# Optimization experiments

Hardware: AMD Instinct MI355X
Metric: run time of the kernel (lower is better)

The kernel has to match this reference:

```python
import jax, jax.numpy as jnp
import numpy as np

B, C, H, W = 8, 256, 64, 64
CQK = C // 8  # query/key channels = 32


def setup_inputs() -> dict:
    key = jax.random.key(0)
    ks = jax.random.split(key, 9)
    s_in = 1.0 / np.sqrt(C)  # conv2d default init scale (kernel_size=1)
    x = jax.random.normal(ks[0], (B, C, H, W), dtype=jnp.float32)
    Wq = jax.random.uniform(ks[1], (CQK, C), jnp.float32, -s_in, s_in)
    bq = jax.random.uniform(ks[2], (CQK,), jnp.float32, -s_in, s_in)
    Wk = jax.random.uniform(ks[3], (CQK, C), jnp.float32, -s_in, s_in)
    bk = jax.random.uniform(ks[4], (CQK,), jnp.float32, -s_in, s_in)
    Wv = jax.random.uniform(ks[5], (C, C), jnp.float32, -s_in, s_in)
    bv = jax.random.uniform(ks[6], (C,), jnp.float32, -s_in, s_in)
    Wf = jax.random.uniform(ks[7], (C, C), jnp.float32, -s_in, s_in)
    bf = jax.random.uniform(ks[8], (C,), jnp.float32, -s_in, s_in)
    return {"x": x, "Wq": Wq, "bq": bq, "Wk": Wk, "bk": bk,
            "Wv": Wv, "bv": bv, "Wf": Wf, "bf": bf}


def reference(x, Wq, bq, Wk, bk, Wv, bv, Wf, bf):
    b, c, h, w = x.shape
    n = h * w
    xf = x.reshape(b, c, n)  # [B, C, N]  (1x1 conv == channel matmul)
    q = jnp.einsum('oc,bcn->bon', Wq, xf) + bq[None, :, None]  # [B, C/8, N]
    k = jnp.einsum('oc,bcn->bon', Wk, xf) + bk[None, :, None]  # [B, C/8, N]
    v = jnp.einsum('oc,bcn->bon', Wv, xf) + bv[None, :, None]  # [B, C, N]
    # energy[b,i,j] = sum_c q[b,c,i] * k[b,c,j]; no scaling (matches source)
    energy = jnp.einsum('bci,bcj->bij', q, k)  # [B, N, N]
    attn = jax.nn.softmax(energy, axis=-1)
    # out[b,c,i] = sum_j v[b,c,j] * attn[b,i,j]
    out = jnp.einsum('bcj,bij->bci', v, attn)  # [B, C, N]
    out = jnp.einsum('oc,bcn->bon', Wf, out) + bf[None, :, None]
    return out.reshape(b, c, h, w)
```

## Files before the change

### kernel.cpp

```cpp
#include <hip/hip_runtime.h>
#include <hip/hip_bf16.h>

#define BATCH 8
#define CCH   256
#define NPOS  4096
#define CQK   32

typedef __attribute__((ext_vector_type(8))) short short8;
typedef __attribute__((ext_vector_type(4))) float f32x4;

__device__ inline unsigned short f2b(float f) {
    __hip_bfloat16 h = __float2bfloat16(f);
    return *reinterpret_cast<unsigned short*>(&h);
}

__device__ inline size_t qk_addr(int b, int n, int c) {
    return ((((size_t)b * 256 + (n >> 4)) * 4 + (c >> 3)) * 16 + (n & 15)) * 8 + (c & 7);
}
__device__ inline size_t v_addr(int b, int c, int j) {
    return (((((size_t)b * 128 + (j >> 5)) * 16 + (c >> 4)) * 4 + ((j >> 3) & 3)) * 16 + (c & 15)) * 8 + (j & 7);
}
__device__ inline size_t wsw_addr(int og, int c, int ol) {
    return ((size_t)(og * 8 + (c >> 5))) * 512 + (((c >> 3) & 3) * 16 + ol) * 8 + (c & 7);
}

__global__ __launch_bounds__(256, 4)
void prep_w_kernel(const float* __restrict__ Wq, const float* __restrict__ Wk,
                   const float* __restrict__ Wv, const float* __restrict__ Wf,
                   unsigned short* __restrict__ wsw)
{
    const int og = blockIdx.x;
    const int t  = threadIdx.x;
    const float* src; int orow;
    if (og < 2)       { src = Wq; orow = og * 16; }
    else if (og < 4)  { src = Wk; orow = (og - 2) * 16; }
    else if (og < 20) { src = Wv; orow = (og - 4) * 16; }
    else              { src = Wf; orow = (og - 20) * 16; }
    #pragma unroll
    for (int e = 0; e < 16; ++e) {
        int idx = t + e * 256;
        int ol = idx >> 8, c = idx & 255;
        wsw[wsw_addr(og, c, ol)] = f2b(src[(orow + ol) * 256 + c]);
    }
}

__global__ __launch_bounds__(512, 2)
void qkv_kernel(const float* __restrict__ x,
                const unsigned short* __restrict__ wsw,
                const float* __restrict__ bq, const float* __restrict__ bk,
                const float* __restrict__ bv,
                unsigned short* __restrict__ qb, unsigned short* __restrict__ kb,
                unsigned short* __restrict__ vb)
{
    __shared__ __align__(16) unsigned short xl[64 * 280];

    const int nt   = blockIdx.x;
    const int b    = blockIdx.y;
    const int t    = threadIdx.x;
    const int w    = t >> 6;
    const int lane = t & 63;
    const int q    = lane >> 4;
    const int ln   = lane & 15;
    const int lofs = (q * 16 + ln) * 8;
    const int wq   = w & 3;
    const int ith  = w >> 2;

    {
        const int c  = t & 255;
        const int nb = (t >> 8) * 4;
        const float* xb = x + ((size_t)(b * 256 + c)) * 4096 + nt * 64;
        #pragma unroll
        for (int e = 0; e < 8; ++e) {
            const int n = nb + e * 8;
            float4 v = *(const float4*)(xb + n);
            xl[(n + 0) * 280 + c] = f2b(v.x);
            xl[(n + 1) * 280 + c] = f2b(v.y);
            xl[(n + 2) * 280 + c] = f2b(v.z);
            xl[(n + 3) * 280 + c] = f2b(v.w);
        }
    }
    __syncthreads();

    short8 wqk[8];
    #pragma unroll
    for (int kk = 0; kk < 8; ++kk)
        wqk[kk] = *(const short8*)(wsw + (size_t)(wq * 8 + kk) * 512 + lofs);
    const float* bias = (wq < 2) ? bq : bk;
    const int cb16 = (wq & 1) * 16;
    const float b0 = bias[cb16 + q * 4 + 0];
    const float b1 = bias[cb16 + q * 4 + 1];
    const float b2 = bias[cb16 + q * 4 + 2];
    const float b3 = bias[cb16 + q * 4 + 3];
    unsigned short* dst = (wq < 2) ? qb : kb;

    #pragma unroll
    for (int itl = 0; itl < 2; ++itl) {
        const int it = ith * 2 + itl;
        short8 xf[8];
        #pragma unroll
        for (int kk = 0; kk < 8; ++kk)
            xf[kk] = *(const short8*)&xl[(it * 16 + ln) * 280 + kk * 32 + q * 8];

        {
            f32x4 acc = {b0, b1, b2, b3};
            #pragma unroll
            for (int kk = 0; kk < 8; ++kk)
                acc = __builtin_amdgcn_mfma_f32_16x16x32_bf16(wqk[kk], xf[kk], acc, 0, 0, 0);
            ushort4 s = {f2b(acc[0]), f2b(acc[1]), f2b(acc[2]), f2b(acc[3])};
            *(ushort4*)(dst + qk_addr(b, nt * 64 + it * 16 + ln, cb16 + q * 4)) = s;
        }

        #pragma unroll
        for (int oq = 0; oq < 4; ++oq) {
            const int c  = wq * 64 + oq * 16 + ln;
            const float bb = bv[c];
            f32x4 acc = {bb, bb, bb, bb};
            const int og = 4 + wq * 4 + oq;
            #pragma unroll
            for (int kk = 0; kk < 8; ++kk) {
                short8 bfr = *(const short8*)(wsw + (size_t)(og * 8 + kk) * 512 + lofs);
                acc = __builtin_amdgcn_mfma_f32_16x16x32_bf16(xf[kk], bfr, acc, 0, 0, 0);
            }
            ushort4 s = {f2b(acc[0]), f2b(acc[1]), f2b(acc[2]), f2b(acc[3])};
            *(ushort4*)(vb + v_addr(b, c, nt * 64 + it * 16 + q * 4)) = s;
        }
    }
}

__global__ __launch_bounds__(256, 2)
void attn_kernel(const unsigned short* __restrict__ qb,
                 const unsigned short* __restrict__ kb,
                 const unsigned short* __restrict__ vb,
                 const unsigned short* __restrict__ wsw,
                 const float* __restrict__ bfb, float* __restrict__ out)
{
    __shared__ __align__(16) unsigned short shbuf[64 * 264];
    __shared__ float lred[64];

    const int bid  = blockIdx.x;
    const int b    = bid & 7;
    const int i0   = (bid >> 3) * 64;
    const int t    = threadIdx.x;
    const int w    = t >> 6;
    const int lane = t & 63;
    const int quad = lane >> 4;
    const int ln   = lane & 15;

    const int ibase = i0 + w * 16;
    const int lofs  = (quad * 16 + ln) * 8;
    const unsigned pswz = (unsigned)((ln & 7) << 4);

    const short8 qfrag = *(const short8*)(qb + (((size_t)b * 256 + (ibase >> 4)) * 512) + lofs);

    f32x4 acc[4][4];
    #pragma unroll
    for (int it = 0; it < 4; ++it)
        #pragma unroll
        for (int cc = 0; cc < 4; ++cc) acc[it][cc] = (f32x4){0.f, 0.f, 0.f, 0.f};
    float accl = 0.f;

    const unsigned short* kbase = kb + (size_t)b * 256 * 512;
    const unsigned short* vbase = vb + (size_t)b * 128 * 8192;

    short8 kf[4], vf[4][2];
    #pragma unroll
    for (int jc = 0; jc < 4; ++jc)
        kf[jc] = *(const short8*)(kbase + (size_t)jc * 512 + lofs);
    #pragma unroll
    for (int cc = 0; cc < 4; ++cc) {
        vf[cc][0] = *(const short8*)(vbase + (w * 4 + cc) * 512 + lofs);
        vf[cc][1] = *(const short8*)(vbase + 8192 + (w * 4 + cc) * 512 + lofs);
    }

    int pb = 0;
    for (int j0 = 0; j0 < 4096; j0 += 64, pb ^= 1) {
        const int jn = (j0 + 64) & 4095;
        short8 kf_n[4], vf_n[4][2];
        #pragma unroll
        for (int jc = 0; jc < 4; ++jc)
            kf_n[jc] = *(const short8*)(kbase + ((size_t)((jn >> 4) + jc) * 512) + lofs);
        const unsigned short* vt_n = vbase + (size_t)(jn >> 5) * 8192;
        #pragma unroll
        for (int cc = 0; cc < 4; ++cc) {
            vf_n[cc][0] = *(const short8*)(vt_n + (w * 4 + cc) * 512 + lofs);
            vf_n[cc][1] = *(const short8*)(vt_n + 8192 + (w * 4 + cc) * 512 + lofs);
        }
        f32x4 st[4];
        #pragma unroll
        for (int jc = 0; jc < 4; ++jc)
            st[jc] = __builtin_amdgcn_mfma_f32_16x16x32_bf16(kf[jc], qfrag,
                      (f32x4){0.f, 0.f, 0.f, 0.f}, 0, 0, 0);
        #pragma unroll
        for (int jc = 0; jc < 4; ++jc) {
            float p0 = __expf(st[jc][0]);
            float p1 = __expf(st[jc][1]);
            float p2 = __expf(st[jc][2]);
            float p3 = __expf(st[jc][3]);
            accl += (p0 + p1) + (p2 + p3);
            ushort4 pk = {f2b(p0), f2b(p1), f2b(p2), f2b(p3)};
            unsigned byt = (((unsigned)(pb * 64 + w * 16 + ln)) << 7)
                         + ((jc * 32 + quad * 8) ^ pswz);
            *(ushort4*)((unsigned char*)shbuf + byt) = pk;
        }
        __syncthreads();
        #pragma unroll
        for (int it = 0; it < 4; ++it) {
            const unsigned rowb = ((unsigned)(pb * 64 + it * 16 + ln)) << 7;
            const short8 pf0 = *(const short8*)((const unsigned char*)shbuf
                                 + rowb + ((quad * 16) ^ pswz));
            const short8 pf1 = *(const short8*)((const unsigned char*)shbuf
                                 + rowb + ((64 + quad * 16) ^ pswz));
            #pragma unroll
            for (int cc = 0; cc < 4; ++cc) {
                acc[it][cc] = __builtin_amdgcn_mfma_f32_16x16x32_bf16(pf0, vf[cc][0], acc[it][cc], 0, 0, 0);
                acc[it][cc] = __builtin_amdgcn_mfma_f32_16x16x32_bf16(pf1, vf[cc][1], acc[it][cc], 0, 0, 0);
            }
        }
        #pragma unroll
        for (int jc = 0; jc < 4; ++jc) kf[jc] = kf_n[jc];
        #pragma unroll
        for (int cc = 0; cc < 4; ++cc) {
            vf[cc][0] = vf_n[cc][0];
            vf[cc][1] = vf_n[cc][1];
        }
    }

    {
        float v = accl;
        v += __shfl_xor(v, 16, 64);
        v += __shfl_xor(v, 32, 64);
        if (lane < 16) lred[w * 16 + lane] = v;
    }
    __syncthreads();

    #pragma unroll
    for (int it = 0; it < 4; ++it) {
        float linv[4];
        #pragma unroll
        for (int r = 0; r < 4; ++r) linv[r] = 1.f / lred[it * 16 + quad * 4 + r];
        #pragma unroll
        for (int cc = 0; cc < 4; ++cc) {
            const int c = w * 64 + cc * 16 + ln;
            #pragma unroll
            for (int r = 0; r < 4; ++r)
                shbuf[((size_t)(it * 16 + quad * 4 + r)) * 264 + c] = f2b(acc[it][cc][r] * linv[r]);
        }
    }
    __syncthreads();

    #pragma unroll
    for (int it = 0; it < 4; ++it) {
        short8 af[8];
        #pragma unroll
        for (int kk = 0; kk < 8; ++kk)
            af[kk] = *(const short8*)&shbuf[((size_t)(it * 16 + ln)) * 264 + kk * 32 + quad * 8];
        #pragma unroll
        for (int oq = 0; oq < 4; ++oq) {
            const int o  = w * 64 + oq * 16 + ln;
            const int og = 20 + w * 4 + oq;
            f32x4 pa = {0.f, 0.f, 0.f, 0.f};
            #pragma unroll
            for (int kk = 0; kk < 8; ++kk) {
                short8 bfr = *(const short8*)(wsw + (size_t)(og * 8 + kk) * 512 + lofs);
                pa = __builtin_amdgcn_mfma_f32_16x16x32_bf16(af[kk], bfr, pa, 0, 0, 0);
            }
            const float bias = bfb[o];
            float4 s = {pa[0] + bias, pa[1] + bias, pa[2] + bias, pa[3] + bias};
            *(float4*)(out + (size_t)(b * 256 + o) * 4096 + i0 + it * 16 + quad * 4) = s;
        }
    }
}

extern "C" void kernel_launch(void* const* d_in, const int* in_sizes, int n_in,
                              void* d_out, int out_size, void* d_ws, size_t ws_size,
                              hipStream_t stream)
{
    const float* x  = (const float*)d_in[0];
    const float* Wq = (const float*)d_in[1];
    const float* bq = (const float*)d_in[2];
    const float* Wk = (const float*)d_in[3];
    const float* bk = (const float*)d_in[4];
    const float* Wv = (const float*)d_in[5];
    const float* bv = (const float*)d_in[6];
    const float* Wf = (const float*)d_in[7];
    const float* bf = (const float*)d_in[8];
    float* out = (float*)d_out;

    unsigned short* qb  = (unsigned short*)d_ws;
    unsigned short* kb  = qb + (size_t)BATCH * NPOS * CQK;
    unsigned short* vb  = kb + (size_t)BATCH * NPOS * CQK;
    unsigned short* wsw = vb + (size_t)BATCH * CCH * NPOS;

    prep_w_kernel<<<36, 256, 0, stream>>>(Wq, Wk, Wv, Wf, wsw);
    qkv_kernel<<<dim3(64, 8), 512, 0, stream>>>(x, wsw, bq, bk, bv, qb, kb, vb);
    attn_kernel<<<512, 256, 0, stream>>>(qb, kb, vb, wsw, bf, out);
}
```

Measured before the change: 203.9 us.

## Fuse weight prep, QKV projection and attention into one persistent kernel with grid barrier

Measured after the change: 334.0 us. 1.64x slower.

```diff
diff --git a/kernel.cpp b/kernel.cpp
--- a/kernel.cpp
+++ b/kernel.cpp
@@ -14,143 +14,138 @@
     return *reinterpret_cast<unsigned short*>(&h);
 }
 
+__device__ inline short8 pack8(float4 a, float4 b) {
+    short8 s;
+    ((unsigned short*)&s)[0] = f2b(a.x);
+    ((unsigned short*)&s)[1] = f2b(a.y);
+    ((unsigned short*)&s)[2] = f2b(a.z);
+    ((unsigned short*)&s)[3] = f2b(a.w);
+    ((unsigned short*)&s)[4] = f2b(b.x);
+    ((unsigned short*)&s)[5] = f2b(b.y);
+    ((unsigned short*)&s)[6] = f2b(b.z);
+    ((unsigned short*)&s)[7] = f2b(b.w);
+    return s;
+}
+
 __device__ inline size_t qk_addr(int b, int n, int c) {
     return ((((size_t)b * 256 + (n >> 4)) * 4 + (c >> 3)) * 16 + (n & 15)) * 8 + (c & 7);
 }
 __device__ inline size_t v_addr(int b, int c, int j) {
     return (((((size_t)b * 128 + (j >> 5)) * 16 + (c >> 4)) * 4 + ((j >> 3) & 3)) * 16 + (c & 15)) * 8 + (j & 7);
 }
-__device__ inline size_t wsw_addr(int og, int c, int ol) {
-    return ((size_t)(og * 8 + (c >> 5))) * 512 + (((c >> 3) & 3) * 16 + ol) * 8 + (c & 7);
-}
-
-__global__ __launch_bounds__(256, 4)
-void prep_w_kernel(const float* __restrict__ Wq, const float* __restrict__ Wk,
-                   const float* __restrict__ Wv, const float* __restrict__ Wf,
-                   unsigned short* __restrict__ wsw)
+
+__global__ __launch_bounds__(256, 2)
+void fused_kernel(const float* __restrict__ x,
+                  const float* __restrict__ Wq, const float* __restrict__ bq,
+                  const float* __restrict__ Wk, const float* __restrict__ bk,
+                  const float* __restrict__ Wv, const float* __restrict__ bv,
+                  const float* __restrict__ Wf, const float* __restrict__ bfb,
+                  unsigned short* __restrict__ kb, unsigned short* __restrict__ vb,
+                  unsigned int* bar, float* __restrict__ out)
 {
-    const int og = blockIdx.x;
-    const int t  = threadIdx.x;
-    const float* src; int orow;
-    if (og < 2)       { src = Wq; orow = og * 16; }
-    else if (og < 4)  { src = Wk; orow = (og - 2) * 16; }
-    else if (og < 20) { src = Wv; orow = (og - 4) * 16; }
-    else              { src = Wf; orow = (og - 20) * 16; }
-    #pragma unroll
-    for (int e = 0; e < 16; ++e) {
-        int idx = t + e * 256;
-        int ol = idx >> 8, c = idx & 255;
-        wsw[wsw_addr(og, c, ol)] = f2b(src[(orow + ol) * 256 + c]);
-    }
-}
-
-__global__ __launch_bounds__(512, 2)
-void qkv_kernel(const float* __restrict__ x,
-                const unsigned short* __restrict__ wsw,
-                const float* __restrict__ bq, const float* __restrict__ bk,
-                const float* __restrict__ bv,
-                unsigned short* __restrict__ qb, unsigned short* __restrict__ kb,
-                unsigned short* __restrict__ vb)
-{
-    __shared__ __align__(16) unsigned short xl[64 * 280];
-
-    const int nt   = blockIdx.x;
-    const int b    = blockIdx.y;
+    __shared__ __align__(16) unsigned short smem[16896];
+    __shared__ __align__(16) unsigned short qlds[2048];
+    __shared__ float lred[64];
+
+    const int bid  = blockIdx.x;
+    const int b    = bid & 7;
+    const int tile = bid >> 3;
     const int t    = threadIdx.x;
     const int w    = t >> 6;
     const int lane = t & 63;
     const int q    = lane >> 4;
     const int ln   = lane & 15;
     const int lofs = (q * 16 + ln) * 8;
-    const int wq   = w & 3;
-    const int ith  = w >> 2;
 
     {
-        const int c  = t & 255;
-        const int nb = (t >> 8) * 4;
-        const float* xb = x + ((size_t)(b * 256 + c)) * 4096 + nt * 64;
-        #pragma unroll
-        for (int e = 0; e < 8; ++e) {
-            const int n = nb + e * 8;
-            float4 v = *(const float4*)(xb + n);
-            xl[(n + 0) * 280 + c] = f2b(v.x);
-            xl[(n + 1) * 280 + c] = f2b(v.y);
-            xl[(n + 2) * 280 + c] = f2b(v.z);
-            xl[(n + 3) * 280 + c] = f2b(v.w);
-        }
-    }
-    __syncthreads();
-
-    short8 wqk[8];
-    #pragma unroll
-    for (int kk = 0; kk < 8; ++kk)
-        wqk[kk] = *(const short8*)(wsw + (size_t)(wq * 8 + kk) * 512 + lofs);
-    const float* bias = (wq < 2) ? bq : bk;
-    const int cb16 = (wq & 1) * 16;
-    const float b0 = bias[cb16 + q * 4 + 0];
-    const float b1 = bias[cb16 + q * 4 + 1];
-    const float b2 = bias[cb16 + q * 4 + 2];
-    const float b3 = bias[cb16 + q * 4 + 3];
-    unsigned short* dst = (wq < 2) ? qb : kb;
-
-    #pragma unroll
-    for (int itl = 0; itl < 2; ++itl) {
-        const int it = ith * 2 + itl;
-        short8 xf[8];
+        const float* xb = x + ((size_t)b * 256) * 4096 + tile * 64;
+        #pragma unroll
+        for (int e = 0; e < 16; ++e) {
+            const int g  = e * 256 + t;
+            const int c  = g >> 4;
+            const int n4 = (g & 15) * 4;
+            float4 v = *(const float4*)(xb + (size_t)c * 4096 + n4);
+            ushort4 s4 = {f2b(v.x), f2b(v.y), f2b(v.z), f2b(v.w)};
+            *(ushort4*)&smem[c * 66 + n4] = s4;
+        }
+        short8 wqk[8];
+        const float* wsrc = ((w < 2) ? Wq : Wk)
+                          + (size_t)((w & 1) * 16 + ln) * 256 + q * 8;
         #pragma unroll
         for (int kk = 0; kk < 8; ++kk)
-            xf[kk] = *(const short8*)&xl[(it * 16 + ln) * 280 + kk * 32 + q * 8];
-
-        {
-            f32x4 acc = {b0, b1, b2, b3};
-            #pragma unroll
-            for (int kk = 0; kk < 8; ++kk)
-                acc = __builtin_amdgcn_mfma_f32_16x16x32_bf16(wqk[kk], xf[kk], acc, 0, 0, 0);
-            ushort4 s = {f2b(acc[0]), f2b(acc[1]), f2b(acc[2]), f2b(acc[3])};
-            *(ushort4*)(dst + qk_addr(b, nt * 64 + it * 16 + ln, cb16 + q * 4)) = s;
-        }
-
-        #pragma unroll
-        for (int oq = 0; oq < 4; ++oq) {
-            const int c  = wq * 64 + oq * 16 + ln;
-            const float bb = bv[c];
-            f32x4 acc = {bb, bb, bb, bb};
-            const int og = 4 + wq * 4 + oq;
-            #pragma unroll
-            for (int kk = 0; kk < 8; ++kk) {
-                short8 bfr = *(const short8*)(wsw + (size_t)(og * 8 + kk) * 512 + lofs);
-                acc = __builtin_amdgcn_mfma_f32_16x16x32_bf16(xf[kk], bfr, acc, 0, 0, 0);
+            wqk[kk] = pack8(*(const float4*)(wsrc + kk * 32),
+                            *(const float4*)(wsrc + kk * 32 + 4));
+        const float* bias = (w < 2) ? bq : bk;
+        const int cb16 = (w & 1) * 16;
+        const float b0 = bias[cb16 + q * 4 + 0];
+        const float b1 = bias[cb16 + q * 4 + 1];
+        const float b2 = bias[cb16 + q * 4 + 2];
+        const float b3 = bias[cb16 + q * 4 + 3];
+        __syncthreads();
+
+        #pragma unroll
+        for (int oqh = 0; oqh < 2; ++oqh) {
+            short8 vwf[2][8];
+            float  bvv[2];
+            #pragma unroll
+            for (int oq2 = 0; oq2 < 2; ++oq2) {
+                const int row = w * 64 + (oqh * 2 + oq2) * 16 + ln;
+                bvv[oq2] = bv[row];
+                const float* vs = Wv + (size_t)row * 256 + q * 8;
+                #pragma unroll
+                for (int kk = 0; kk < 8; ++kk)
+                    vwf[oq2][kk] = pack8(*(const float4*)(vs + kk * 32),
+                                         *(const float4*)(vs + kk * 32 + 4));
             }
-            ushort4 s = {f2b(acc[0]), f2b(acc[1]), f2b(acc[2]), f2b(acc[3])};
-            *(ushort4*)(vb + v_addr(b, c, nt * 64 + it * 16 + q * 4)) = s;
-        }
-    }
-}
-
-__global__ __launch_bounds__(256, 2)
-void attn_kernel(const unsigned short* __restrict__ qb,
-                 const unsigned short* __restrict__ kb,
-                 const unsigned short* __restrict__ vb,
-                 const unsigned short* __restrict__ wsw,
-                 const float* __restrict__ bfb, float* __restrict__ out)
-{
-    __shared__ __align__(16) unsigned short shbuf[64 * 264];
-    __shared__ float lred[64];
-
-    const int bid  = blockIdx.x;
-    const int b    = bid & 7;
-    const int i0   = (bid >> 3) * 64;
-    const int t    = threadIdx.x;
-    const int w    = t >> 6;
-    const int lane = t & 63;
-    const int quad = lane >> 4;
-    const int ln   = lane & 15;
-
-    const int ibase = i0 + w * 16;
-    const int lofs  = (quad * 16 + ln) * 8;
+            #pragma unroll
+            for (int it = 0; it < 4; ++it) {
+                short8 xf[8];
+                #pragma unroll
+                for (int kk = 0; kk < 8; ++kk) {
+                    short8 s;
+                    #pragma unroll
+                    for (int j = 0; j < 8; ++j)
+                        ((unsigned short*)&s)[j] = smem[(kk * 32 + q * 8 + j) * 66 + it * 16 + ln];
+                    xf[kk] = s;
+                }
+                if (oqh == 0) {
+                    f32x4 acc = {b0, b1, b2, b3};
+                    #pragma unroll
+                    for (int kk = 0; kk < 8; ++kk)
+                        acc = __builtin_amdgcn_mfma_f32_16x16x32_bf16(wqk[kk], xf[kk], acc, 0, 0, 0);
+                    ushort4 s = {f2b(acc[0]), f2b(acc[1]), f2b(acc[2]), f2b(acc[3])};
+                    if (w < 2)
+                        *(ushort4*)(qlds + qk_addr(0, it * 16 + ln, cb16 + q * 4)) = s;
+                    else
+                        *(ushort4*)(kb + qk_addr(b, tile * 64 + it * 16 + ln, cb16 + q * 4)) = s;
+                }
+                #pragma unroll
+                for (int oq2 = 0; oq2 < 2; ++oq2) {
+                    const int c = w * 64 + (oqh * 2 + oq2) * 16 + ln;
+                    f32x4 acc = {bvv[oq2], bvv[oq2], bvv[oq2], bvv[oq2]};
+                    #pragma unroll
+                    for (int kk = 0; kk < 8; ++kk)
+                        acc = __builtin_amdgcn_mfma_f32_16x16x32_bf16(xf[kk], vwf[oq2][kk], acc, 0, 0, 0);
+                    ushort4 s = {f2b(acc[0]), f2b(acc[1]), f2b(acc[2]), f2b(acc[3])};
+                    *(ushort4*)(vb + v_addr(b, c, tile * 64 + it * 16 + q * 4)) = s;
+                }
+            }
+        }
+    }
+
+    __threadfence();
+    __syncthreads();
+    if (t == 0) {
+        atomicAdd(bar, 1u);
+        while (atomicAdd(bar, 0u) < 512u) __builtin_amdgcn_s_sleep(8);
+    }
+    __syncthreads();
+    __threadfence();
+
+    const int i0   = tile * 64;
     const unsigned pswz = (unsigned)((ln & 7) << 4);
 
-    const short8 qfrag = *(const short8*)(qb + (((size_t)b * 256 + (ibase >> 4)) * 512) + lofs);
+    const short8 qfrag = *(const short8*)(qlds + (size_t)w * 512 + lofs);
 
     f32x4 acc[4][4];
     #pragma unroll
@@ -199,17 +194,17 @@
             accl += (p0 + p1) + (p2 + p3);
             ushort4 pk = {f2b(p0), f2b(p1), f2b(p2), f2b(p3)};
             unsigned byt = (((unsigned)(pb * 64 + w * 16 + ln)) << 7)
-                         + ((jc * 32 + quad * 8) ^ pswz);
-            *(ushort4*)((unsigned char*)shbuf + byt) = pk;
+                         + ((jc * 32 + q * 8) ^ pswz);
+            *(ushort4*)((unsigned char*)smem + byt) = pk;
         }
         __syncthreads();
         #pragma unroll
         for (int it = 0; it < 4; ++it) {
             const unsigned rowb = ((unsigned)(pb * 64 + it * 16 + ln)) << 7;
-            const short8 pf0 = *(const short8*)((const unsigned char*)shbuf
-                                 + rowb + ((quad * 16) ^ pswz));
-            const short8 pf1 = *(const short8*)((const unsigned char*)shbuf
-                                 + rowb + ((64 + quad * 16) ^ pswz));
+            const short8 pf0 = *(const short8*)((const unsigned char*)smem
+                                 + rowb + ((q * 16) ^ pswz));
+            const short8 pf1 = *(const short8*)((const unsigned char*)smem
+                                 + rowb + ((64 + q * 16) ^ pswz));
             #pragma unroll
             for (int cc = 0; cc < 4; ++cc) {
                 acc[it][cc] = __builtin_amdgcn_mfma_f32_16x16x32_bf16(pf0, vf[cc][0], acc[it][cc], 0, 0, 0);
@@ -237,36 +232,39 @@
     for (int it = 0; it < 4; ++it) {
         float linv[4];
         #pragma unroll
-        for (int r = 0; r < 4; ++r) linv[r] = 1.f / lred[it * 16 + quad * 4 + r];
+        for (int r = 0; r < 4; ++r) linv[r] = 1.f / lred[it * 16 + q * 4 + r];
         #pragma unroll
         for (int cc = 0; cc < 4; ++cc) {
             const int c = w * 64 + cc * 16 + ln;
             #pragma unroll
             for (int r = 0; r < 4; ++r)
-                shbuf[((size_t)(it * 16 + quad * 4 + r)) * 264 + c] = f2b(acc[it][cc][r] * linv[r]);
-        }
-    }
-    __syncthreads();
-
-    #pragma unroll
-    for (int it = 0; it < 4; ++it) {
-        short8 af[8];
+                smem[((size_t)(it * 16 + q * 4 + r)) * 264 + c] = f2b(acc[it][cc][r] * linv[r]);
+        }
+    }
+    __syncthreads();
+
+    #pragma unroll
+    for (int oq = 0; oq < 4; ++oq) {
+        const int o = w * 64 + oq * 16 + ln;
+        short8 wff[8];
+        const float* fs = Wf + (size_t)o * 256 + q * 8;
         #pragma unroll
         for (int kk = 0; kk < 8; ++kk)
-            af[kk] = *(const short8*)&shbuf[((size_t)(it * 16 + ln)) * 264 + kk * 32 + quad * 8];
-        #pragma unroll
-        for (int oq = 0; oq < 4; ++oq) {
-            const int o  = w * 64 + oq * 16 + ln;
-            const int og = 20 + w * 4 + oq;
+            wff[kk] = pack8(*(const float4*)(fs + kk * 32),
+                            *(const float4*)(fs + kk * 32 + 4));
+        const float bias = bfb[o];
+        #pragma unroll
+        for (int it = 0; it < 4; ++it) {
+            short8 af[8];
+            #pragma unroll
+            for (int kk = 0; kk < 8; ++kk)
+                af[kk] = *(const short8*)&smem[((size_t)(it * 16 + ln)) * 264 + kk * 32 + q * 8];
             f32x4 pa = {0.f, 0.f, 0.f, 0.f};
             #pragma unroll
-            for (int kk = 0; kk < 8; ++kk) {
-                short8 bfr = *(const short8*)(wsw + (size_t)(og * 8 + kk) * 512 + lofs);
-                pa = __builtin_amdgcn_mfma_f32_16x16x32_bf16(af[kk], bfr, pa, 0, 0, 0);
-            }
-            const float bias = bfb[o];
+            for (int kk = 0; kk < 8; ++kk)
+                pa = __builtin_amdgcn_mfma_f32_16x16x32_bf16(af[kk], wff[kk], pa, 0, 0, 0);
             float4 s = {pa[0] + bias, pa[1] + bias, pa[2] + bias, pa[3] + bias};
-            *(float4*)(out + (size_t)(b * 256 + o) * 4096 + i0 + it * 16 + quad * 4) = s;
+            *(float4*)(out + (size_t)(b * 256 + o) * 4096 + i0 + it * 16 + q * 4) = s;
         }
     }
 }
@@ -286,12 +284,11 @@
     const float* bf = (const float*)d_in[8];
     float* out = (float*)d_out;
 
-    unsigned short* qb  = (unsigned short*)d_ws;
-    unsigned short* kb  = qb + (size_t)BATCH * NPOS * CQK;
+    unsigned int*   bar = (unsigned int*)d_ws;
+    unsigned short* kb  = (unsigned short*)d_ws + 64;
     unsigned short* vb  = kb + (size_t)BATCH * NPOS * CQK;
-    unsigned short* wsw = vb + (size_t)BATCH * CCH * NPOS;
-
-    prep_w_kernel<<<36, 256, 0, stream>>>(Wq, Wk, Wv, Wf, wsw);
-    qkv_kernel<<<dim3(64, 8), 512, 0, stream>>>(x, wsw, bq, bk, bv, qb, kb, vb);
-    attn_kernel<<<512, 256, 0, stream>>>(qb, kb, vb, wsw, bf, out);
-}
+
+    hipMemsetAsync(bar, 0, 8, stream);
+    fused_kernel<<<512, 256, 0, stream>>>(x, Wq, bq, Wk, bk, Wv, bv, Wf, bf,
+                                          kb, vb, bar, out);
+}
```

## Software-pipeline attention loop: overlap next tile's softmax with current PV MFMAs

Applied to the files above, without the earlier changes.

New measurement: 213.1 us. +4.5%, slower.

```diff
diff --git a/kernel.cpp b/kernel.cpp
--- a/kernel.cpp
+++ b/kernel.cpp
@@ -5,6 +5,7 @@
 #define CCH   256
 #define NPOS  4096
 #define CQK   32
+#define LOG2E 1.4426950408889634f
 
 typedef __attribute__((ext_vector_type(8))) short short8;
 typedef __attribute__((ext_vector_type(4))) float f32x4;
@@ -31,16 +32,16 @@
 {
     const int og = blockIdx.x;
     const int t  = threadIdx.x;
-    const float* src; int orow;
+    const float* src; int orow; float scl = 1.f;
     if (og < 2)       { src = Wq; orow = og * 16; }
-    else if (og < 4)  { src = Wk; orow = (og - 2) * 16; }
+    else if (og < 4)  { src = Wk; orow = (og - 2) * 16; scl = LOG2E; }
     else if (og < 20) { src = Wv; orow = (og - 4) * 16; }
     else              { src = Wf; orow = (og - 20) * 16; }
     #pragma unroll
     for (int e = 0; e < 16; ++e) {
         int idx = t + e * 256;
         int ol = idx >> 8, c = idx & 255;
-        wsw[wsw_addr(og, c, ol)] = f2b(src[(orow + ol) * 256 + c]);
+        wsw[wsw_addr(og, c, ol)] = f2b(src[(orow + ol) * 256 + c] * scl);
     }
 }
 
@@ -86,11 +87,12 @@
     for (int kk = 0; kk < 8; ++kk)
         wqk[kk] = *(const short8*)(wsw + (size_t)(wq * 8 + kk) * 512 + lofs);
     const float* bias = (wq < 2) ? bq : bk;
+    const float ksc = (wq < 2) ? 1.f : LOG2E;
     const int cb16 = (wq & 1) * 16;
-    const float b0 = bias[cb16 + q * 4 + 0];
-    const float b1 = bias[cb16 + q * 4 + 1];
-    const float b2 = bias[cb16 + q * 4 + 2];
-    const float b3 = bias[cb16 + q * 4 + 3];
+    const float b0 = bias[cb16 + q * 4 + 0] * ksc;
+    const float b1 = bias[cb16 + q * 4 + 1] * ksc;
+    const float b2 = bias[cb16 + q * 4 + 2] * ksc;
+    const float b3 = bias[cb16 + q * 4 + 3] * ksc;
     unsigned short* dst = (wq < 2) ? qb : kb;
 
     #pragma unroll
@@ -162,47 +164,55 @@
     const unsigned short* kbase = kb + (size_t)b * 256 * 512;
     const unsigned short* vbase = vb + (size_t)b * 128 * 8192;
 
-    short8 kf[4], vf[4][2];
+    short8 kfB[4], kfC[4], vfA[4][2], vfB[4][2];
     #pragma unroll
     for (int jc = 0; jc < 4; ++jc)
-        kf[jc] = *(const short8*)(kbase + (size_t)jc * 512 + lofs);
+        kfC[jc] = *(const short8*)(kbase + (size_t)jc * 512 + lofs);
     #pragma unroll
     for (int cc = 0; cc < 4; ++cc) {
-        vf[cc][0] = *(const short8*)(vbase + (w * 4 + cc) * 512 + lofs);
-        vf[cc][1] = *(const short8*)(vbase + 8192 + (w * 4 + cc) * 512 + lofs);
-    }
+        vfA[cc][0] = *(const short8*)(vbase + (w * 4 + cc) * 512 + lofs);
+        vfA[cc][1] = *(const short8*)(vbase + 8192 + (w * 4 + cc) * 512 + lofs);
+    }
+    #pragma unroll
+    for (int jc = 0; jc < 4; ++jc)
+        kfB[jc] = *(const short8*)(kbase + (size_t)(4 + jc) * 512 + lofs);
+
+    #pragma unroll
+    for (int jc = 0; jc < 4; ++jc) {
+        f32x4 st = __builtin_amdgcn_mfma_f32_16x16x32_bf16(kfC[jc], qfrag,
+                    (f32x4){0.f, 0.f, 0.f, 0.f}, 0, 0, 0);
+        float p0 = exp2f(st[0]);
+        float p1 = exp2f(st[1]);
+        float p2 = exp2f(st[2]);
+        float p3 = exp2f(st[3]);
+        accl += (p0 + p1) + (p2 + p3);
+        ushort4 pk = {f2b(p0), f2b(p1), f2b(p2), f2b(p3)};
+        unsigned byt = (((unsigned)(w * 16 + ln)) << 7)
+                     + ((jc * 32 + quad * 8) ^ pswz);
+        *(ushort4*)((unsigned char*)shbuf + byt) = pk;
+    }
+    __syncthreads();
 
     int pb = 0;
-    for (int j0 = 0; j0 < 4096; j0 += 64, pb ^= 1) {
-        const int jn = (j0 + 64) & 4095;
-        short8 kf_n[4], vf_n[4][2];
+    for (int j0 = 0; j0 < 4032; j0 += 64, pb ^= 1) {
+        const int jn1 = j0 + 64;
+        const int jn2 = (j0 + 128) & 4095;
+        const unsigned short* vt = vbase + (size_t)(jn1 >> 5) * 8192;
+        #pragma unroll
+        for (int cc = 0; cc < 4; ++cc) {
+            vfB[cc][0] = *(const short8*)(vt + (w * 4 + cc) * 512 + lofs);
+            vfB[cc][1] = *(const short8*)(vt + 8192 + (w * 4 + cc) * 512 + lofs);
+        }
         #pragma unroll
         for (int jc = 0; jc < 4; ++jc)
-            kf_n[jc] = *(const short8*)(kbase + ((size_t)((jn >> 4) + jc) * 512) + lofs);
-        const unsigned short* vt_n = vbase + (size_t)(jn >> 5) * 8192;
-        #pragma unroll
-        for (int cc = 0; cc < 4; ++cc) {
-            vf_n[cc][0] = *(const short8*)(vt_n + (w * 4 + cc) * 512 + lofs);
-            vf_n[cc][1] = *(const short8*)(vt_n + 8192 + (w * 4 + cc) * 512 + lofs);
-        }
-        f32x4 st[4];
+            kfC[jc] = *(const short8*)(kbase + ((size_t)((jn2 >> 4) + jc) * 512) + lofs);
+
+        __builtin_amdgcn_s_setprio(1);
+        f32x4 stB[4];
         #pragma unroll
         for (int jc = 0; jc < 4; ++jc)
-            st[jc] = __builtin_amdgcn_mfma_f32_16x16x32_bf16(kf[jc], qfrag,
-                      (f32x4){0.f, 0.f, 0.f, 0.f}, 0, 0, 0);
-        #pragma unroll
-        for (int jc = 0; jc < 4; ++jc) {
-            float p0 = __expf(st[jc][0]);
-            float p1 = __expf(st[jc][1]);
-            float p2 = __expf(st[jc][2]);
-            float p3 = __expf(st[jc][3]);
-            accl += (p0 + p1) + (p2 + p3);
-            ushort4 pk = {f2b(p0), f2b(p1), f2b(p2), f2b(p3)};
-            unsigned byt = (((unsigned)(pb * 64 + w * 16 + ln)) << 7)
-                         + ((jc * 32 + quad * 8) ^ pswz);
-            *(ushort4*)((unsigned char*)shbuf + byt) = pk;
-        }
-        __syncthreads();
+            stB[jc] = __builtin_amdgcn_mfma_f32_16x16x32_bf16(kfB[jc], qfrag,
+                       (f32x4){0.f, 0.f, 0.f, 0.f}, 0, 0, 0);
         #pragma unroll
         for (int it = 0; it < 4; ++it) {
             const unsigned rowb = ((unsigned)(pb * 64 + it * 16 + ln)) << 7;
@@ -212,16 +222,44 @@
                                  + rowb + ((64 + quad * 16) ^ pswz));
             #pragma unroll
             for (int cc = 0; cc < 4; ++cc) {
-                acc[it][cc] = __builtin_amdgcn_mfma_f32_16x16x32_bf16(pf0, vf[cc][0], acc[it][cc], 0, 0, 0);
-                acc[it][cc] = __builtin_amdgcn_mfma_f32_16x16x32_bf16(pf1, vf[cc][1], acc[it][cc], 0, 0, 0);
+                acc[it][cc] = __builtin_amdgcn_mfma_f32_16x16x32_bf16(pf0, vfA[cc][0], acc[it][cc], 0, 0, 0);
+                acc[it][cc] = __builtin_amdgcn_mfma_f32_16x16x32_bf16(pf1, vfA[cc][1], acc[it][cc], 0, 0, 0);
             }
         }
-        #pragma unroll
-        for (int jc = 0; jc < 4; ++jc) kf[jc] = kf_n[jc];
+        __builtin_amdgcn_s_setprio(0);
+        #pragma unroll
+        for (int jc = 0; jc < 4; ++jc) {
+            float p0 = exp2f(stB[jc][0]);
+            float p1 = exp2f(stB[jc][1]);
+            float p2 = exp2f(stB[jc][2]);
+            float p3 = exp2f(stB[jc][3]);
+            accl += (p0 + p1) + (p2 + p3);
+            ushort4 pk = {f2b(p0), f2b(p1), f2b(p2), f2b(p3)};
+            unsigned byt = (((unsigned)((pb ^ 1) * 64 + w * 16 + ln)) << 7)
+                         + ((jc * 32 + quad * 8) ^ pswz);
+            *(ushort4*)((unsigned char*)shbuf + byt) = pk;
+        }
+        __syncthreads();
+        #pragma unroll
+        for (int jc = 0; jc < 4; ++jc) kfB[jc] = kfC[jc];
         #pragma unroll
         for (int cc = 0; cc < 4; ++cc) {
-            vf[cc][0] = vf_n[cc][0];
-            vf[cc][1] = vf_n[cc][1];
+            vfA[cc][0] = vfB[cc][0];
+            vfA[cc][1] = vfB[cc][1];
+        }
+    }
+
+    #pragma unroll
+    for (int it = 0; it < 4; ++it) {
+        const unsigned rowb = ((unsigned)(pb * 64 + it * 16 + ln)) << 7;
+        const short8 pf0 = *(const short8*)((const unsigned char*)shbuf
+                             + rowb + ((quad * 16) ^ pswz));
+        const short8 pf1 = *(const short8*)((const unsigned char*)shbuf
+                             + rowb + ((64 + quad * 16) ^ pswz));
+        #pragma unroll
+        for (int cc = 0; cc < 4; ++cc) {
+            acc[it][cc] = __builtin_amdgcn_mfma_f32_16x16x32_bf16(pf0, vfA[cc][0], acc[it][cc], 0, 0, 0);
+            acc[it][cc] = __builtin_amdgcn_mfma_f32_16x16x32_bf16(pf1, vfA[cc][1], acc[it][cc], 0, 0, 0);
         }
     }
 
```
